# Performance work log

Hardware: AMD Instinct MI355X
Metric: run time of the kernel (lower is better)

## Reference

```python
import jax, jax.numpy as jnp
import numpy as np

D_MODEL = 1024
N_HEADS = 16
D_HEAD = 64


def setup_inputs() -> dict:
    key = jax.random.key(0)
    ks = jax.random.split(key, 5)
    B, T = 2, 2048
    scale = 1.0 / np.sqrt(D_MODEL)
    x = jax.random.normal(ks[0], (B, T, D_MODEL), dtype=jnp.float32)
    Wq = jax.random.normal(ks[1], (N_HEADS * D_HEAD, D_MODEL), dtype=jnp.float32) * scale
    Wk = jax.random.normal(ks[2], (N_HEADS * D_HEAD, D_MODEL), dtype=jnp.float32) * scale
    Wv = jax.random.normal(ks[3], (N_HEADS * D_HEAD, D_MODEL), dtype=jnp.float32) * scale
    Wo = jax.random.normal(ks[4], (D_MODEL, N_HEADS * D_HEAD), dtype=jnp.float32) * scale
    return {"x": x, "Wq": Wq, "Wk": Wk, "Wv": Wv, "Wo": Wo}


def reference(x, Wq, Wk, Wv, Wo):
    B, T, D = x.shape
    # Linear(y = x @ W.T), then split heads: [B, H, T, d]
    def split_heads(y):
        return y.reshape(B, T, N_HEADS, D_HEAD).transpose(0, 2, 1, 3)
    q = split_heads(x @ Wq.T)
    k = split_heads(x @ Wk.T)
    v = split_heads(x @ Wv.T)
    scale = D_HEAD ** -0.5
    # Materialized [B, H, T, T] scores, as in the original module
    scores = jnp.einsum('bhtd,bhTd->bhtT', q, k) * scale
    attn = jax.nn.softmax(scores, axis=-1)
    y = jnp.einsum('bhtT,bhTd->bhtd', attn, v)
    y = y.transpose(0, 2, 1, 3).reshape(B, T, N_HEADS * D_HEAD)
    return y @ Wo.T
```

## Files before the change

### kernel.cpp

```cpp
#include <hip/hip_runtime.h>
#include <hip/hip_bf16.h>

typedef __attribute__((ext_vector_type(8))) short bf16x8;
typedef __attribute__((ext_vector_type(4))) float f32x4;
typedef unsigned short u16t;

#define DEVINL static __device__ __forceinline__

DEVINL u16t f2bf(float f) {
  union { __hip_bfloat16 h; u16t u; } cv;
  cv.h = __float2bfloat16(f);
  return cv.u;
}

DEVINL u16t f2bf_fast(float f) {
  union { float f; unsigned u; } c;
  c.f = f;
  return (u16t)((c.u + 0x8000u) >> 16);
}

DEVINL void async16(void* lds, const void* g) {
  __builtin_amdgcn_global_load_lds((const __attribute__((address_space(1))) void*)g,
                                   (__attribute__((address_space(3))) void*)lds,
                                   16, 0, 0);
}

__global__ __launch_bounds__(256) void convert_bf16(
    const float* __restrict__ x,  const float* __restrict__ wq,
    const float* __restrict__ wk, const float* __restrict__ wv,
    const float* __restrict__ wo,
    u16t* __restrict__ xb, u16t* __restrict__ wqb, u16t* __restrict__ wkb,
    u16t* __restrict__ wvb, u16t* __restrict__ wob) {
  const int blk = blockIdx.x;
  const float* src; u16t* dst; size_t off;
  if (blk < 4096)      { src = x;  dst = xb;  off = (size_t)blk * 1024; }
  else if (blk < 5120) { src = wq; dst = wqb; off = (size_t)(blk - 4096) * 1024; }
  else if (blk < 6144) { src = wk; dst = wkb; off = (size_t)(blk - 5120) * 1024; }
  else if (blk < 7168) { src = wv; dst = wvb; off = (size_t)(blk - 6144) * 1024; }
  else                 { src = wo; dst = wob; off = (size_t)(blk - 7168) * 1024; }
  const size_t i = off + (size_t)threadIdx.x * 4;
  const float4 v = *(const float4*)&src[i];
  ushort4 r;
  r.x = f2bf(v.x); r.y = f2bf(v.y); r.z = f2bf(v.z); r.w = f2bf(v.w);
  *(ushort4*)&dst[i] = r;
}

template <int MODE>
__global__ __launch_bounds__(256) void gemm_bt(
    const u16t* __restrict__ A, const u16t* __restrict__ B,
    void* __restrict__ C0, void* __restrict__ C1, void* __restrict__ C2,
    int M, int N, int K) {
  __shared__ u16t As[2][128 * 32];
  __shared__ u16t Bs[2][128 * 32];

  const int tid = threadIdx.x;
  const int lane = tid & 63;
  const int w = tid >> 6;
  const int wm = w >> 1, wn = w & 1;
  const int quad = lane >> 4, cl = lane & 15;
  const int m0 = blockIdx.y * 128;
  const int n0 = blockIdx.x * 128;

  const int srow = lane >> 2;
  const int scol = (lane & 3) * 8;

  f32x4 acc[4][4] = {};

  for (int k0 = 0; k0 < K; k0 += 64) {
    __syncthreads();
    #pragma unroll
    for (int p = 0; p < 2; ++p)
      #pragma unroll
      for (int ii = 0; ii < 2; ++ii) {
        const int c = w + ii * 4;
        async16(&As[p][c * 512], &A[(size_t)(m0 + c * 16 + srow) * K + k0 + p * 32 + scol]);
        async16(&Bs[p][c * 512], &B[(size_t)(n0 + c * 16 + srow) * K + k0 + p * 32 + scol]);
      }
    __syncthreads();
    #pragma unroll
    for (int p = 0; p < 2; ++p) {
      bf16x8 af[4], bfr[4];
      #pragma unroll
      for (int i = 0; i < 4; ++i)
        af[i] = *(const bf16x8*)&As[p][(wm * 64 + i * 16 + cl) * 32 + quad * 8];
      #pragma unroll
      for (int j = 0; j < 4; ++j)
        bfr[j] = *(const bf16x8*)&Bs[p][(wn * 64 + j * 16 + cl) * 32 + quad * 8];
      #pragma unroll
      for (int i = 0; i < 4; ++i)
        #pragma unroll
        for (int j = 0; j < 4; ++j)
          acc[i][j] = __builtin_amdgcn_mfma_f32_16x16x32_bf16(af[i], bfr[j], acc[i][j], 0, 0, 0);
    }
  }

  const int nz = n0 >> 10;
  #pragma unroll
  for (int i = 0; i < 4; ++i)
    #pragma unroll
    for (int j = 0; j < 4; ++j) {
      const int mb = m0 + wm * 64 + i * 16 + quad * 4;
      const int n  = n0 + wn * 64 + j * 16 + cl;
      if (MODE == 0) {
        #pragma unroll
        for (int r = 0; r < 4; ++r)
          ((float*)C0)[(size_t)(mb + r) * N + n] = acc[i][j][r];
      } else {
        const int nw = n & 1023, h = nw >> 6, d = nw & 63;
        const int b = mb >> 11, tb = mb & 2047;
        const size_t bh = (size_t)(b * 16 + h);
        if (nz == 2) {
          ushort4 v4;
          v4.x = f2bf(acc[i][j][0]); v4.y = f2bf(acc[i][j][1]);
          v4.z = f2bf(acc[i][j][2]); v4.w = f2bf(acc[i][j][3]);
          const size_t addr = (bh << 17) +
              (size_t)(((d >> 4) * 256 + (tb >> 3)) * 128 + (d & 15) * 8 + (tb & 7));
          *(ushort4*)&((u16t*)C2)[addr] = v4;
        } else if (nz == 1) {
          const size_t basea = (bh << 17) +
              (size_t)(((tb >> 4) * 8 + (d >> 3)) * 128 + (d & 7));
          #pragma unroll
          for (int r = 0; r < 4; ++r)
            ((u16t*)C1)[basea + ((tb & 15) + r) * 8] = f2bf(acc[i][j][r]);
        } else {
          #pragma unroll
          for (int r = 0; r < 4; ++r)
            ((u16t*)C0)[(bh * 2048 + tb + r) * 64 + d] =
                f2bf(acc[i][j][r] * 0.18033688011112043f);
        }
      }
    }
}

__global__ __launch_bounds__(256) void flash_attn(
    const u16t* __restrict__ Q, const u16t* __restrict__ Kt,
    const u16t* __restrict__ Vt, u16t* __restrict__ Y) {
  __shared__ u16t Ps[4 * 16 * 136];

  const int tid = threadIdx.x;
  const int lane = tid & 63;
  const int w = tid >> 6;
  const int quad = lane >> 4, cl = lane & 15;
  const int bh = blockIdx.y;
  const int q0 = blockIdx.x * 64;
  const u16t* Kb = Kt + ((size_t)bh << 17);
  const u16t* Vb = Vt + ((size_t)bh << 17);

  bf16x8 aq[2];
  #pragma unroll
  for (int ks = 0; ks < 2; ++ks)
    aq[ks] = *(const bf16x8*)&Q[((size_t)bh * 2048 + q0 + w * 16 + cl) * 64 + ks * 32 + quad * 8];

  f32x4 o[4] = {};
  float lsum[4] = {0.f, 0.f, 0.f, 0.f};

  u16t* Pw = &Ps[w * 16 * 136];

  for (int jt = 0; jt < 16; ++jt) {
    const int j0 = jt * 128;

    f32x4 s[8] = {};
    #pragma unroll
    for (int ks = 0; ks < 2; ++ks) {
      bf16x8 kf[8];
      #pragma unroll
      for (int js = 0; js < 8; ++js)
        kf[js] = *(const bf16x8*)&Kb[(size_t)((((j0 >> 4) + js) * 8 + ks * 4) * 128) + lane * 8];
      #pragma unroll
      for (int js = 0; js < 8; ++js)
        s[js] = __builtin_amdgcn_mfma_f32_16x16x32_bf16(aq[ks], kf[js], s[js], 0, 0, 0);
    }

    #pragma unroll
    for (int js = 0; js < 8; ++js)
      #pragma unroll
      for (int r = 0; r < 4; ++r) {
        const float p = __builtin_exp2f(s[js][r]);
        lsum[r] += p;
        Pw[(quad * 4 + r) * 136 + js * 16 + cl] = f2bf_fast(p);
      }

    #pragma unroll
    for (int ks = 0; ks < 4; ++ks) {
      const bf16x8 ap = *(const bf16x8*)&Pw[cl * 136 + ks * 32 + quad * 8];
      bf16x8 vf[4];
      #pragma unroll
      for (int ds = 0; ds < 4; ++ds)
        vf[ds] = *(const bf16x8*)&Vb[(size_t)((ds * 256 + (j0 >> 3) + ks * 4) * 128) + lane * 8];
      #pragma unroll
      for (int ds = 0; ds < 4; ++ds)
        o[ds] = __builtin_amdgcn_mfma_f32_16x16x32_bf16(ap, vf[ds], o[ds], 0, 0, 0);
    }
  }

  #pragma unroll
  for (int r = 0; r < 4; ++r) {
    #pragma unroll
    for (int msk = 1; msk < 16; msk <<= 1) lsum[r] += __shfl_xor(lsum[r], msk, 64);
  }

  const int b = bh >> 4, h = bh & 15;
  #pragma unroll
  for (int ds = 0; ds < 4; ++ds)
    #pragma unroll
    for (int r = 0; r < 4; ++r) {
      const int t = q0 + w * 16 + quad * 4 + r;
      const int d = ds * 16 + cl;
      Y[((size_t)b * 2048 + t) * 1024 + h * 64 + d] = f2bf(o[ds][r] / lsum[r]);
    }
}

extern "C" void kernel_launch(void* const* d_in, const int* in_sizes, int n_in,
                              void* d_out, int out_size, void* d_ws, size_t ws_size,
                              hipStream_t stream) {
  (void)in_sizes; (void)n_in; (void)out_size; (void)ws_size;
  const float* x  = (const float*)d_in[0];
  const float* Wq = (const float*)d_in[1];
  const float* Wk = (const float*)d_in[2];
  const float* Wv = (const float*)d_in[3];
  const float* Wo = (const float*)d_in[4];

  char* ws = (char*)d_ws;
  const size_t MB = 1024 * 1024;
  u16t* xb  = (u16t*)(ws);
  u16t* Wqb = (u16t*)(ws + 8 * MB);
  u16t* Wkb = (u16t*)(ws + 10 * MB);
  u16t* Wvb = (u16t*)(ws + 12 * MB);
  u16t* Wob = (u16t*)(ws + 14 * MB);
  u16t* Qw  = (u16t*)(ws + 16 * MB);
  u16t* Ktw = (u16t*)(ws + 24 * MB);
  u16t* Vtw = (u16t*)(ws + 32 * MB);
  u16t* Yw  = xb;

  convert_bf16<<<8192, 256, 0, stream>>>(x, Wq, Wk, Wv, Wo, xb, Wqb, Wkb, Wvb, Wob);
  gemm_bt<1><<<dim3(24, 32), 256, 0, stream>>>(
      xb, Wqb, Qw, Ktw, Vtw, 4096, 3072, 1024);
  flash_attn<<<dim3(32, 32), 256, 0, stream>>>(Qw, Ktw, Vtw, Yw);
  gemm_bt<0><<<dim3(8, 32), 256, 0, stream>>>(
      Yw, Wob, d_out, d_out, d_out, 4096, 1024, 1024);
}
```

Baseline: 212.9 us.

## Transpose score MFMA, pack bf16 P stores, compute row sums via MFMA

Swaps the QK^T MFMA operands so each lane holds four consecutive keys for one query. P can then be converted with v_cvt_pk_bf16 and written to LDS as 8-byte stores instead of scalar 16-bit stores. Softmax row sums are accumulated with an extra MFMA of P against a ones vector, replacing per-element VALU adds and the final cross-lane shuffles. The normalization uses a reciprocal multiply. This trades some VALU and LDS-store work for one extra MFMA per k-step, and the sums now use bf16-rounded P values.

```diff
diff --git a/kernel.cpp b/kernel.cpp
--- a/kernel.cpp
+++ b/kernel.cpp
@@ -13,10 +13,10 @@
   return cv.u;
 }
 
-DEVINL u16t f2bf_fast(float f) {
-  union { float f; unsigned u; } c;
-  c.f = f;
-  return (u16t)((c.u + 0x8000u) >> 16);
+DEVINL unsigned cvt_pk_bf16(float a, float b) {
+  unsigned r;
+  asm("v_cvt_pk_bf16_f32 %0, %1, %2" : "=v"(r) : "v"(a), "v"(b));
+  return r;
 }
 
 DEVINL void async16(void* lds, const void* g) {
@@ -151,8 +151,12 @@
   for (int ks = 0; ks < 2; ++ks)
     aq[ks] = *(const bf16x8*)&Q[((size_t)bh * 2048 + q0 + w * 16 + cl) * 64 + ks * 32 + quad * 8];
 
+  bf16x8 onesf;
+  #pragma unroll
+  for (int i = 0; i < 8; ++i) onesf[i] = (short)0x3F80;
+
   f32x4 o[4] = {};
-  float lsum[4] = {0.f, 0.f, 0.f, 0.f};
+  f32x4 psum = {};
 
   u16t* Pw = &Ps[w * 16 * 136];
 
@@ -168,17 +172,16 @@
         kf[js] = *(const bf16x8*)&Kb[(size_t)((((j0 >> 4) + js) * 8 + ks * 4) * 128) + lane * 8];
       #pragma unroll
       for (int js = 0; js < 8; ++js)
-        s[js] = __builtin_amdgcn_mfma_f32_16x16x32_bf16(aq[ks], kf[js], s[js], 0, 0, 0);
-    }
-
-    #pragma unroll
-    for (int js = 0; js < 8; ++js)
-      #pragma unroll
-      for (int r = 0; r < 4; ++r) {
-        const float p = __builtin_exp2f(s[js][r]);
-        lsum[r] += p;
-        Pw[(quad * 4 + r) * 136 + js * 16 + cl] = f2bf_fast(p);
-      }
+        s[js] = __builtin_amdgcn_mfma_f32_16x16x32_bf16(kf[js], aq[ks], s[js], 0, 0, 0);
+    }
+
+    #pragma unroll
+    for (int js = 0; js < 8; ++js) {
+      uint2 pk;
+      pk.x = cvt_pk_bf16(__builtin_exp2f(s[js][0]), __builtin_exp2f(s[js][1]));
+      pk.y = cvt_pk_bf16(__builtin_exp2f(s[js][2]), __builtin_exp2f(s[js][3]));
+      *(uint2*)&Pw[cl * 136 + js * 16 + quad * 4] = pk;
+    }
 
     #pragma unroll
     for (int ks = 0; ks < 4; ++ks) {
@@ -187,17 +190,16 @@
       #pragma unroll
       for (int ds = 0; ds < 4; ++ds)
         vf[ds] = *(const bf16x8*)&Vb[(size_t)((ds * 256 + (j0 >> 3) + ks * 4) * 128) + lane * 8];
+      psum = __builtin_amdgcn_mfma_f32_16x16x32_bf16(ap, onesf, psum, 0, 0, 0);
       #pragma unroll
       for (int ds = 0; ds < 4; ++ds)
         o[ds] = __builtin_amdgcn_mfma_f32_16x16x32_bf16(ap, vf[ds], o[ds], 0, 0, 0);
     }
   }
 
-  #pragma unroll
-  for (int r = 0; r < 4; ++r) {
-    #pragma unroll
-    for (int msk = 1; msk < 16; msk <<= 1) lsum[r] += __shfl_xor(lsum[r], msk, 64);
-  }
+  float inv[4];
+  #pragma unroll
+  for (int r = 0; r < 4; ++r) inv[r] = __builtin_amdgcn_rcpf(psum[r]);
 
   const int b = bh >> 4, h = bh & 15;
   #pragma unroll
@@ -206,7 +208,7 @@
     for (int r = 0; r < 4; ++r) {
       const int t = q0 + w * 16 + quad * 4 + r;
       const int d = ds * 16 + cl;
-      Y[((size_t)b * 2048 + t) * 1024 + h * 64 + d] = f2bf(o[ds][r] / lsum[r]);
+      Y[((size_t)b * 2048 + t) * 1024 + h * 64 + d] = f2bf(o[ds][r] * inv[r]);
     }
 }
 
```

After: 208.6 us. 2.0% less time.
